# Optimization experiments

Measured on AMD Instinct MI355X. Metric: run time of the kernel, lower is better.

## Reference

```python
import jax, jax.numpy as jnp
import numpy as np

HASH_CODE_LEN = 8  # config['hash_code_len']
EPS = 1e-12

def _l2norm(x):
    n = jnp.sqrt(jnp.sum(x * x, axis=-1, keepdims=True))
    return x / jnp.maximum(n, EPS)

def setup_inputs() -> dict:
    key = jax.random.key(0)
    k1, k2, k3, k4 = jax.random.split(key, 4)
    B, H, S, D = 2, 12, 2048, 64
    Q = jax.random.normal(k1, (B, H, S, D), dtype=jnp.float32)
    K = jax.random.normal(k2, (B, H, S, D), dtype=jnp.float32)
    V = jax.random.normal(k3, (B, H, S, D), dtype=jnp.float32)
    mask = jnp.ones((B, S), dtype=jnp.float32)
    conv_w = jax.random.normal(k4, (H, 1, 3, 1), dtype=jnp.float32)  # depthwise Conv2d weight [H,1,w,1]
    return {"Q": Q, "K": K, "V": V, "mask": mask, "conv_w": conv_w}

def reference(Q, K, V, mask, conv_w):
    B, H, S, D = Q.shape
    # conv branch: depthwise conv over the sequence axis, per head (groups=num_head)
    Vm = V * mask[:, None, :, None]  # [B,H,S,D]
    conv_V = jax.lax.conv_general_dilated(
        Vm, conv_w,
        window_strides=(1, 1),
        padding=[(1, 1), (0, 0)],  # (conv_window//2, 0)
        dimension_numbers=("NCHW", "OIHW", "NCHW"),
        feature_group_count=H,
    )
    # YOSO attention: exact expectation of LSH cumulation.
    # collision prob of unit vectors q,k over hash_code_len bits: (1 - acos(q.k)/pi)^tau
    qn = _l2norm(Q)
    kn = _l2norm(K)
    dots = jnp.einsum("bhsd,bhtd->bhst", qn, kn)
    dots = jnp.clip(dots, -1.0, 1.0)
    W = (1.0 - jnp.arccos(dots) / jnp.pi) ** HASH_CODE_LEN  # [B,H,S,S]
    W = W * mask[:, None, None, :]  # key mask
    X = jnp.einsum("bhst,bhtd->bhsd", W, V)
    X = X * mask[:, None, :, None]  # query mask
    X = _l2norm(X)  # kernel.normalize(X)
    return X + conv_V
```

## Files before the change

### kernel.cpp

```cpp
#include <hip/hip_runtime.h>
#include <hip/hip_bf16.h>
#include <math.h>

#define NB 2
#define NH 12
#define NS 2048
#define ND 64
#define NBH (NB * NH)
#define TILE_USHORT 4096
#define QK_BLOCKS 6144
#define V_BLOCKS (NBH * 32)

typedef __attribute__((ext_vector_type(8))) short short8;
typedef __attribute__((ext_vector_type(4))) float floatx4;
typedef __attribute__((ext_vector_type(2))) float float2v;

__device__ __forceinline__ unsigned short f32_to_bf16_rne(float f) {
  unsigned int u = __float_as_uint(f);
  u += 0x7fffu + ((u >> 16) & 1u);
  return (unsigned short)(u >> 16);
}

__device__ __forceinline__ unsigned int pack_bf16_trunc(float lo, float hi) {
  return __builtin_amdgcn_perm(__float_as_uint(hi), __float_as_uint(lo), 0x07060302);
}

__device__ __forceinline__ float2v mk2(float x) { return (float2v){x, x}; }
__device__ __forceinline__ float2v max2(float2v a, float2v b) {
  return (float2v){fmaxf(a[0], b[0]), fmaxf(a[1], b[1])};
}
__device__ __forceinline__ float2v abs2(float2v a) {
  return (float2v){fabsf(a[0]), fabsf(a[1])};
}

__device__ __forceinline__ float yoso_f_exact(float d) {
  const float c0 = 0.49996030f;
  const float c1 = -0.06751822f;
  const float c2 = 0.02363774f;
  const float c3 = -0.00596174f;
  float a = fminf(fabsf(d), 1.0f);
  float p = fmaf(fmaf(fmaf(c3, a, c2), a, c1), a, c0);
  float u = sqrtf(1.0f - a) * p;
  return (d >= 0.0f) ? (1.0f - u) : u;
}

__device__ __forceinline__ void gload_lds16(const unsigned short* src,
                                            unsigned short* lds_dst) {
  __builtin_amdgcn_global_load_lds(
      (const __attribute__((address_space(1))) unsigned int*)(const void*)src,
      (__attribute__((address_space(3))) unsigned int*)(void*)lds_dst,
      16, 0, 0);
}

__global__ __launch_bounds__(256) void prep_all(
    const float* __restrict__ Q, const float* __restrict__ K,
    const float* __restrict__ V, const float* __restrict__ mask,
    unsigned short* __restrict__ qimg, unsigned short* __restrict__ kimg,
    unsigned short* __restrict__ vimg) {
  int blk = blockIdx.x;
  if (blk < QK_BLOCKS) {
    int row = blk * 16 + (threadIdx.x >> 4);
    int li  = threadIdx.x & 15;
    const float* src = Q;
    unsigned short* dst = qimg;
    if (row >= NBH * NS) { src = K; dst = kimg; row -= NBH * NS; }
    float4 v = *(const float4*)(src + (size_t)row * ND + li * 4);
    float ss = v.x * v.x + v.y * v.y + v.z * v.z + v.w * v.w;
    ss += __shfl_xor(ss, 1, 64);
    ss += __shfl_xor(ss, 2, 64);
    ss += __shfl_xor(ss, 4, 64);
    ss += __shfl_xor(ss, 8, 64);
    float rn = 1.0f / fmaxf(sqrtf(ss), 1e-12f);
    ushort4 o;
    o.x = f32_to_bf16_rne(v.x * rn);
    o.y = f32_to_bf16_rne(v.y * rn);
    o.z = f32_to_bf16_rne(v.z * rn);
    o.w = f32_to_bf16_rne(v.w * rn);
    int bh = row >> 11;
    int s  = row & (NS - 1);
    int kt = s >> 6, r = s & 63;
    int frag = (li >> 3) * 4 + (r >> 4);
    int ln   = ((li >> 1) & 3) * 16 + (r & 15);
    size_t off = (size_t)(bh * 32 + kt) * TILE_USHORT + frag * 512 + ln * 8 + (li & 1) * 4;
    *(ushort4*)(dst + off) = o;
  } else {
    int vb = blk - QK_BLOCKS;
    int bh = vb >> 5, kt = vb & 31, t0 = kt * 64;
    int b  = bh / NH;
    __shared__ float sT[64][65];
    int tid = threadIdx.x;
    int tr = tid >> 2;
    int dc = (tid & 3) * 16;
    float m = mask[b * NS + t0 + tr];
    const float* vp = V + ((size_t)bh * NS + t0 + tr) * ND + dc;
    #pragma unroll
    for (int jj = 0; jj < 16; jj += 4) {
      float4 v = *(const float4*)(vp + jj);
      sT[dc + jj + 0][tr] = v.x * m;
      sT[dc + jj + 1][tr] = v.y * m;
      sT[dc + jj + 2][tr] = v.z * m;
      sT[dc + jj + 3][tr] = v.w * m;
    }
    __syncthreads();
    int dr = tid >> 2;
    unsigned short* op = vimg + (size_t)(bh * 32 + kt) * TILE_USHORT;
    #pragma unroll
    for (int g = 0; g < 2; ++g) {
      int combo = (tid & 3) * 2 + g;
      int kk2 = combo >> 2;
      int qd  = combo & 3;
      uint4 u;
      int tb = kk2 * 32 + qd * 4;
      u.x = (unsigned int)f32_to_bf16_rne(sT[dr][tb + 0]) |
            ((unsigned int)f32_to_bf16_rne(sT[dr][tb + 1]) << 16);
      u.y = (unsigned int)f32_to_bf16_rne(sT[dr][tb + 2]) |
            ((unsigned int)f32_to_bf16_rne(sT[dr][tb + 3]) << 16);
      u.z = (unsigned int)f32_to_bf16_rne(sT[dr][tb + 16]) |
            ((unsigned int)f32_to_bf16_rne(sT[dr][tb + 17]) << 16);
      u.w = (unsigned int)f32_to_bf16_rne(sT[dr][tb + 18]) |
            ((unsigned int)f32_to_bf16_rne(sT[dr][tb + 19]) << 16);
      int frag = kk2 * 4 + (dr >> 4);
      int ln   = qd * 16 + (dr & 15);
      *(uint4*)(op + frag * 512 + ln * 8) = u;
    }
  }
}

__global__ __launch_bounds__(256, 4) void yoso_main(
    const unsigned short* __restrict__ qimg, const unsigned short* __restrict__ kimg,
    const unsigned short* __restrict__ vimg, const float* __restrict__ V,
    const float* __restrict__ mask, const float* __restrict__ conv_w,
    float* __restrict__ out) {
  int bid = blockIdx.x;
  int lid = (bid & 7) * 96 + (bid >> 3);
  int bh = lid >> 5;
  int b  = bh / NH;
  int h  = bh % NH;
  int qt = lid & 31;
  int s0 = qt * 64;

  __shared__ unsigned short stage[2][8192];

  int tid  = threadIdx.x;
  int wv   = tid >> 6;
  int lane = tid & 63;
  int lq   = lane & 15;
  int quad = lane >> 4;

  uint4 qfrag[2];
  {
    const unsigned short* qtile = qimg + (size_t)(bh * 32 + qt) * TILE_USHORT;
    #pragma unroll
    for (int kk = 0; kk < 2; ++kk)
      qfrag[kk] = *(const uint4*)(qtile + (kk * 4 + wv) * 512 + lane * 8);
  }

  float w0 = conv_w[h * 3 + 0], w1 = conv_w[h * 3 + 1], w2 = conv_w[h * 3 + 2];

  floatx4 acc[4];
  #pragma unroll
  for (int fd = 0; fd < 4; ++fd) acc[fd] = (floatx4){0.f, 0.f, 0.f, 0.f};

  const unsigned short* kb  = kimg + (size_t)bh * 32 * TILE_USHORT;
  const unsigned short* vbI = vimg + (size_t)bh * 32 * TILE_USHORT;

  const float P0 = 0.3183098862f;
  const float P1 = 0.0530516477f;
  const float P2 = 0.0238732415f;
  const float P3 = 0.0142098402f;
  const float P4 = 0.0096701727f;
  const float P5 = 0.0071212906f;

  auto stage_tile = [&](int buf, int kt) {
    const unsigned short* ksrc = kb  + (size_t)kt * TILE_USHORT;
    const unsigned short* vsrc = vbI + (size_t)kt * TILE_USHORT;
    #pragma unroll
    for (int c = 0; c < 4; ++c) {
      int region = wv * 4 + c;
      const unsigned short* src = (region < 8) ? (ksrc + region * 512)
                                               : (vsrc + (region - 8) * 512);
      gload_lds16(src + lane * 8, &stage[buf][region * 512]);
    }
  };

  auto compute_tile = [&](const unsigned short* sbuf) {
    uint4 kf[2][4];
    #pragma unroll
    for (int kk = 0; kk < 2; ++kk)
      #pragma unroll
      for (int ft = 0; ft < 4; ++ft)
        kf[kk][ft] = *(const uint4*)(sbuf + (kk * 4 + ft) * 512 + lane * 8);

    floatx4 sc[4];
    #pragma unroll
    for (int ft = 0; ft < 4; ++ft) sc[ft] = (floatx4){0.f, 0.f, 0.f, 0.f};
    #pragma unroll
    for (int kk = 0; kk < 2; ++kk) {
      short8 bq = *(const short8*)&qfrag[kk];
      #pragma unroll
      for (int ft = 0; ft < 4; ++ft)
        sc[ft] = __builtin_amdgcn_mfma_f32_16x16x32_bf16(
            *(const short8*)&kf[kk][ft], bq, sc[ft], 0, 0, 0);
    }

    uint4 vf[2][4];
    #pragma unroll
    for (int kk2 = 0; kk2 < 2; ++kk2)
      #pragma unroll
      for (int fd = 0; fd < 4; ++fd)
        vf[kk2][fd] = *(const uint4*)(sbuf + 4096 + (kk2 * 4 + fd) * 512 + lane * 8);

    {
      float2v mxy = mk2(0.f);
      #pragma unroll
      for (int ft = 0; ft < 4; ++ft) {
        float2v* p = (float2v*)&sc[ft];
        mxy = max2(mxy, max2(abs2(p[0]), abs2(p[1])));
      }
      float mx = fmaxf(mxy[0], mxy[1]);
      if (__builtin_expect(__any(mx > 0.82f), 0)) {
        #pragma unroll
        for (int ft = 0; ft < 4; ++ft)
          #pragma unroll
          for (int r = 0; r < 4; ++r) {
            float f = yoso_f_exact(sc[ft][r]);
            float f2 = f * f;
            float f4 = f2 * f2;
            sc[ft][r] = f4 * f4;
          }
      } else {
        float2v c5 = mk2(P5), c4 = mk2(P4), c3 = mk2(P3), c2 = mk2(P2),
                c1 = mk2(P1), c0 = mk2(P0), hf = mk2(0.5f);
        #pragma unroll
        for (int ft = 0; ft < 4; ++ft) {
          float2v* p = (float2v*)&sc[ft];
          #pragma unroll
          for (int hh = 0; hh < 2; ++hh) {
            float2v d = p[hh];
            float2v y = d * d;
            float2v pp = ((((c5 * y + c4) * y + c3) * y + c2) * y + c1) * y + c0;
            float2v f = pp * d + hf;
            float2v f2 = f * f;
            float2v f4 = f2 * f2;
            p[hh] = f4 * f4;
          }
        }
      }
    }

    #pragma unroll
    for (int kk2 = 0; kk2 < 2; ++kk2) {
      uint4 u;
      u.x = pack_bf16_trunc(sc[2 * kk2][0], sc[2 * kk2][1]);
      u.y = pack_bf16_trunc(sc[2 * kk2][2], sc[2 * kk2][3]);
      u.z = pack_bf16_trunc(sc[2 * kk2 + 1][0], sc[2 * kk2 + 1][1]);
      u.w = pack_bf16_trunc(sc[2 * kk2 + 1][2], sc[2 * kk2 + 1][3]);
      short8 bw = *(short8*)&u;
      #pragma unroll
      for (int fd = 0; fd < 4; ++fd)
        acc[fd] = __builtin_amdgcn_mfma_f32_16x16x32_bf16(
            *(const short8*)&vf[kk2][fd], bw, acc[fd], 0, 0, 0);
    }
  };

  stage_tile(0, 0);
  __syncthreads();
  #pragma unroll 1
  for (int ss = 0; ss < 16; ++ss) {
    int kt = ss * 2;
    stage_tile(1, kt + 1);
    compute_tile(stage[0]);
    __syncthreads();
    if (ss < 15) stage_tile(0, kt + 2);
    compute_tile(stage[1]);
    __syncthreads();
  }

  int s = s0 + wv * 16 + lq;
  float qm  = mask[b * NS + s];
  float qm0 = (s > 0) ? mask[b * NS + s - 1] : 0.f;
  float qm2 = (s < NS - 1) ? mask[b * NS + s + 1] : 0.f;
  float ssum = 0.f;
  #pragma unroll
  for (int fd = 0; fd < 4; ++fd)
    #pragma unroll
    for (int r = 0; r < 4; ++r) {
      float x = acc[fd][r] * qm;
      acc[fd][r] = x;
      ssum += x * x;
    }
  ssum += __shfl_xor(ssum, 16, 64);
  ssum += __shfl_xor(ssum, 32, 64);
  float rn = 1.0f / fmaxf(sqrtf(ssum), 1e-12f);

  const float* vfull = V + ((size_t)bh * NS + s) * ND;
  #pragma unroll
  for (int fd = 0; fd < 4; ++fd) {
    int d = fd * 16 + quad * 4;
    float4 vc1 = *(const float4*)(vfull + d);
    float4 cv;
    cv.x = w1 * vc1.x * qm; cv.y = w1 * vc1.y * qm;
    cv.z = w1 * vc1.z * qm; cv.w = w1 * vc1.w * qm;
    if (s > 0) {
      float4 vc0 = *(const float4*)(vfull - ND + d);
      cv.x += w0 * vc0.x * qm0; cv.y += w0 * vc0.y * qm0;
      cv.z += w0 * vc0.z * qm0; cv.w += w0 * vc0.w * qm0;
    }
    if (s < NS - 1) {
      float4 vc2 = *(const float4*)(vfull + ND + d);
      cv.x += w2 * vc2.x * qm2; cv.y += w2 * vc2.y * qm2;
      cv.z += w2 * vc2.z * qm2; cv.w += w2 * vc2.w * qm2;
    }
    float4 o;
    o.x = acc[fd][0] * rn + cv.x;
    o.y = acc[fd][1] * rn + cv.y;
    o.z = acc[fd][2] * rn + cv.z;
    o.w = acc[fd][3] * rn + cv.w;
    *(float4*)(out + ((size_t)bh * NS + s) * ND + d) = o;
  }
}

extern "C" void kernel_launch(void* const* d_in, const int* in_sizes, int n_in,
                              void* d_out, int out_size, void* d_ws, size_t ws_size,
                              hipStream_t stream) {
  const float* Q      = (const float*)d_in[0];
  const float* K      = (const float*)d_in[1];
  const float* V      = (const float*)d_in[2];
  const float* mask   = (const float*)d_in[3];
  const float* conv_w = (const float*)d_in[4];
  float* out = (float*)d_out;

  const size_t seg = (size_t)NBH * NS * ND * sizeof(unsigned short);
  unsigned short* qimg = (unsigned short*)d_ws;
  unsigned short* kimg = (unsigned short*)((char*)d_ws + seg);
  unsigned short* vimg = (unsigned short*)((char*)d_ws + 2 * seg);

  prep_all<<<QK_BLOCKS + V_BLOCKS, 256, 0, stream>>>(Q, K, V, mask, qimg, kimg, vimg);
  yoso_main<<<NBH * 32, 256, 0, stream>>>(qimg, kimg, vimg, V, mask, conv_w, out);
}
```

Before: 142.5 us.

## Split key tiles across wave pairs and read V fragments directly from global

Work is repartitioned so each wave handles two 16-row query fragments and half of the key tiles, with the two key-parity halves reduced through shared memory at the end. Only K is staged into LDS, two tiles at a time. V fragments are now loaded straight from global memory instead of through LDS. The aim is to reuse each K fragment across two query fragments and halve the number of loop-iteration barriers. The cost is higher register pressure (launch bounds lowered from 4 to 3 blocks per CU), uncoalesced-latency exposure on the direct V loads, and an extra cross-wave reduction in the epilogue.

```diff
diff --git a/kernel.cpp b/kernel.cpp
--- a/kernel.cpp
+++ b/kernel.cpp
@@ -126,7 +126,7 @@
   }
 }
 
-__global__ __launch_bounds__(256, 4) void yoso_main(
+__global__ __launch_bounds__(256, 3) void yoso_main(
     const unsigned short* __restrict__ qimg, const unsigned short* __restrict__ kimg,
     const unsigned short* __restrict__ vimg, const float* __restrict__ V,
     const float* __restrict__ mask, const float* __restrict__ conv_w,
@@ -139,27 +139,33 @@
   int qt = lid & 31;
   int s0 = qt * 64;
 
-  __shared__ unsigned short stage[2][8192];
+  __shared__ unsigned short kbuf[4][4096];
 
   int tid  = threadIdx.x;
   int wv   = tid >> 6;
   int lane = tid & 63;
   int lq   = lane & 15;
   int quad = lane >> 4;
-
-  uint4 qfrag[2];
+  int qs   = wv & 1;
+  int kp   = wv >> 1;
+
+  uint4 qfrag[2][2];
   {
     const unsigned short* qtile = qimg + (size_t)(bh * 32 + qt) * TILE_USHORT;
     #pragma unroll
-    for (int kk = 0; kk < 2; ++kk)
-      qfrag[kk] = *(const uint4*)(qtile + (kk * 4 + wv) * 512 + lane * 8);
+    for (int j = 0; j < 2; ++j)
+      #pragma unroll
+      for (int kk = 0; kk < 2; ++kk)
+        qfrag[j][kk] = *(const uint4*)(qtile + (kk * 4 + qs * 2 + j) * 512 + lane * 8);
   }
 
   float w0 = conv_w[h * 3 + 0], w1 = conv_w[h * 3 + 1], w2 = conv_w[h * 3 + 2];
 
-  floatx4 acc[4];
+  floatx4 acc[2][4];
   #pragma unroll
-  for (int fd = 0; fd < 4; ++fd) acc[fd] = (floatx4){0.f, 0.f, 0.f, 0.f};
+  for (int j = 0; j < 2; ++j)
+    #pragma unroll
+    for (int fd = 0; fd < 4; ++fd) acc[j][fd] = (floatx4){0.f, 0.f, 0.f, 0.f};
 
   const unsigned short* kb  = kimg + (size_t)bh * 32 * TILE_USHORT;
   const unsigned short* vbI = vimg + (size_t)bh * 32 * TILE_USHORT;
@@ -171,152 +177,193 @@
   const float P4 = 0.0096701727f;
   const float P5 = 0.0071212906f;
 
-  auto stage_tile = [&](int buf, int kt) {
-    const unsigned short* ksrc = kb  + (size_t)kt * TILE_USHORT;
-    const unsigned short* vsrc = vbI + (size_t)kt * TILE_USHORT;
+  auto stage_pair = [&](int pb, int t0) {
     #pragma unroll
     for (int c = 0; c < 4; ++c) {
       int region = wv * 4 + c;
-      const unsigned short* src = (region < 8) ? (ksrc + region * 512)
-                                               : (vsrc + (region - 8) * 512);
-      gload_lds16(src + lane * 8, &stage[buf][region * 512]);
+      int tsel   = region >> 3;
+      int piece  = region & 7;
+      gload_lds16(kb + (size_t)(t0 + tsel) * TILE_USHORT + piece * 512 + lane * 8,
+                  &kbuf[pb + tsel][piece * 512]);
     }
   };
 
-  auto compute_tile = [&](const unsigned short* sbuf) {
+  stage_pair(0, 0);
+  __syncthreads();
+
+  #pragma unroll 1
+  for (int r = 0; r < 16; ++r) {
+    int pb = (r & 1) * 2;
+    if (r < 15) stage_pair(2 - pb, 2 * r + 2);
+
+    int kt = 2 * r + kp;
+    const unsigned short* sb = kbuf[pb + kp];
+
     uint4 kf[2][4];
     #pragma unroll
     for (int kk = 0; kk < 2; ++kk)
       #pragma unroll
       for (int ft = 0; ft < 4; ++ft)
-        kf[kk][ft] = *(const uint4*)(sbuf + (kk * 4 + ft) * 512 + lane * 8);
-
-    floatx4 sc[4];
-    #pragma unroll
-    for (int ft = 0; ft < 4; ++ft) sc[ft] = (floatx4){0.f, 0.f, 0.f, 0.f};
+        kf[kk][ft] = *(const uint4*)(sb + (kk * 4 + ft) * 512 + lane * 8);
+
+    floatx4 sc[2][4];
+    #pragma unroll
+    for (int j = 0; j < 2; ++j)
+      #pragma unroll
+      for (int ft = 0; ft < 4; ++ft) sc[j][ft] = (floatx4){0.f, 0.f, 0.f, 0.f};
     #pragma unroll
     for (int kk = 0; kk < 2; ++kk) {
-      short8 bq = *(const short8*)&qfrag[kk];
-      #pragma unroll
-      for (int ft = 0; ft < 4; ++ft)
-        sc[ft] = __builtin_amdgcn_mfma_f32_16x16x32_bf16(
-            *(const short8*)&kf[kk][ft], bq, sc[ft], 0, 0, 0);
-    }
-
+      #pragma unroll
+      for (int j = 0; j < 2; ++j) {
+        short8 bq = *(const short8*)&qfrag[j][kk];
+        #pragma unroll
+        for (int ft = 0; ft < 4; ++ft)
+          sc[j][ft] = __builtin_amdgcn_mfma_f32_16x16x32_bf16(
+              *(const short8*)&kf[kk][ft], bq, sc[j][ft], 0, 0, 0);
+      }
+    }
+
+    const unsigned short* vtile = vbI + (size_t)kt * TILE_USHORT;
     uint4 vf[2][4];
     #pragma unroll
     for (int kk2 = 0; kk2 < 2; ++kk2)
       #pragma unroll
       for (int fd = 0; fd < 4; ++fd)
-        vf[kk2][fd] = *(const uint4*)(sbuf + 4096 + (kk2 * 4 + fd) * 512 + lane * 8);
+        vf[kk2][fd] = *(const uint4*)(vtile + (kk2 * 4 + fd) * 512 + lane * 8);
 
     {
       float2v mxy = mk2(0.f);
       #pragma unroll
-      for (int ft = 0; ft < 4; ++ft) {
-        float2v* p = (float2v*)&sc[ft];
-        mxy = max2(mxy, max2(abs2(p[0]), abs2(p[1])));
-      }
+      for (int j = 0; j < 2; ++j)
+        #pragma unroll
+        for (int ft = 0; ft < 4; ++ft) {
+          float2v* p = (float2v*)&sc[j][ft];
+          mxy = max2(mxy, max2(abs2(p[0]), abs2(p[1])));
+        }
       float mx = fmaxf(mxy[0], mxy[1]);
       if (__builtin_expect(__any(mx > 0.82f), 0)) {
         #pragma unroll
-        for (int ft = 0; ft < 4; ++ft)
+        for (int j = 0; j < 2; ++j)
           #pragma unroll
-          for (int r = 0; r < 4; ++r) {
-            float f = yoso_f_exact(sc[ft][r]);
-            float f2 = f * f;
-            float f4 = f2 * f2;
-            sc[ft][r] = f4 * f4;
-          }
+          for (int ft = 0; ft < 4; ++ft)
+            #pragma unroll
+            for (int r2 = 0; r2 < 4; ++r2) {
+              float f = yoso_f_exact(sc[j][ft][r2]);
+              float f2 = f * f;
+              float f4 = f2 * f2;
+              sc[j][ft][r2] = f4 * f4;
+            }
       } else {
         float2v c5 = mk2(P5), c4 = mk2(P4), c3 = mk2(P3), c2 = mk2(P2),
                 c1 = mk2(P1), c0 = mk2(P0), hf = mk2(0.5f);
         #pragma unroll
-        for (int ft = 0; ft < 4; ++ft) {
-          float2v* p = (float2v*)&sc[ft];
+        for (int j = 0; j < 2; ++j)
           #pragma unroll
-          for (int hh = 0; hh < 2; ++hh) {
-            float2v d = p[hh];
-            float2v y = d * d;
-            float2v pp = ((((c5 * y + c4) * y + c3) * y + c2) * y + c1) * y + c0;
-            float2v f = pp * d + hf;
-            float2v f2 = f * f;
-            float2v f4 = f2 * f2;
-            p[hh] = f4 * f4;
+          for (int ft = 0; ft < 4; ++ft) {
+            float2v* p = (float2v*)&sc[j][ft];
+            #pragma unroll
+            for (int hh = 0; hh < 2; ++hh) {
+              float2v d = p[hh];
+              float2v y = d * d;
+              float2v pp = ((((c5 * y + c4) * y + c3) * y + c2) * y + c1) * y + c0;
+              float2v f = pp * d + hf;
+              float2v f2 = f * f;
+              float2v f4 = f2 * f2;
+              p[hh] = f4 * f4;
+            }
           }
+      }
+    }
+
+    #pragma unroll
+    for (int j = 0; j < 2; ++j) {
+      #pragma unroll
+      for (int kk2 = 0; kk2 < 2; ++kk2) {
+        uint4 u;
+        u.x = pack_bf16_trunc(sc[j][2 * kk2][0], sc[j][2 * kk2][1]);
+        u.y = pack_bf16_trunc(sc[j][2 * kk2][2], sc[j][2 * kk2][3]);
+        u.z = pack_bf16_trunc(sc[j][2 * kk2 + 1][0], sc[j][2 * kk2 + 1][1]);
+        u.w = pack_bf16_trunc(sc[j][2 * kk2 + 1][2], sc[j][2 * kk2 + 1][3]);
+        short8 bw = *(short8*)&u;
+        #pragma unroll
+        for (int fd = 0; fd < 4; ++fd)
+          acc[j][fd] = __builtin_amdgcn_mfma_f32_16x16x32_bf16(
+              *(const short8*)&vf[kk2][fd], bw, acc[j][fd], 0, 0, 0);
+      }
+    }
+
+    __syncthreads();
+  }
+
+  float* xch = (float*)&kbuf[0][0];
+  if (kp == 1) {
+    #pragma unroll
+    for (int j = 0; j < 2; ++j) {
+      float* wr = xch + (qs * 2 + j) * 1088;
+      #pragma unroll
+      for (int fd = 0; fd < 4; ++fd)
+        #pragma unroll
+        for (int r2 = 0; r2 < 4; ++r2)
+          wr[lq * 68 + fd * 16 + quad * 4 + r2] = acc[j][fd][r2];
+    }
+  }
+  __syncthreads();
+  if (kp == 0) {
+    #pragma unroll
+    for (int j = 0; j < 2; ++j) {
+      const float* rd = xch + (qs * 2 + j) * 1088;
+      #pragma unroll
+      for (int fd = 0; fd < 4; ++fd)
+        #pragma unroll
+        for (int r2 = 0; r2 < 4; ++r2)
+          acc[j][fd][r2] += rd[lq * 68 + fd * 16 + quad * 4 + r2];
+    }
+
+    #pragma unroll
+    for (int j = 0; j < 2; ++j) {
+      int s = s0 + qs * 32 + j * 16 + lq;
+      float qm  = mask[b * NS + s];
+      float qm0 = (s > 0) ? mask[b * NS + s - 1] : 0.f;
+      float qm2 = (s < NS - 1) ? mask[b * NS + s + 1] : 0.f;
+      float ssum = 0.f;
+      #pragma unroll
+      for (int fd = 0; fd < 4; ++fd)
+        #pragma unroll
+        for (int r2 = 0; r2 < 4; ++r2) {
+          float x = acc[j][fd][r2] * qm;
+          acc[j][fd][r2] = x;
+          ssum += x * x;
         }
+      ssum += __shfl_xor(ssum, 16, 64);
+      ssum += __shfl_xor(ssum, 32, 64);
+      float rn = 1.0f / fmaxf(sqrtf(ssum), 1e-12f);
+
+      const float* vfull = V + ((size_t)bh * NS + s) * ND;
+      #pragma unroll
+      for (int fd = 0; fd < 4; ++fd) {
+        int d = fd * 16 + quad * 4;
+        float4 vc1 = *(const float4*)(vfull + d);
+        float4 cv;
+        cv.x = w1 * vc1.x * qm; cv.y = w1 * vc1.y * qm;
+        cv.z = w1 * vc1.z * qm; cv.w = w1 * vc1.w * qm;
+        if (s > 0) {
+          float4 vc0 = *(const float4*)(vfull - ND + d);
+          cv.x += w0 * vc0.x * qm0; cv.y += w0 * vc0.y * qm0;
+          cv.z += w0 * vc0.z * qm0; cv.w += w0 * vc0.w * qm0;
+        }
+        if (s < NS - 1) {
+          float4 vc2 = *(const float4*)(vfull + ND + d);
+          cv.x += w2 * vc2.x * qm2; cv.y += w2 * vc2.y * qm2;
+          cv.z += w2 * vc2.z * qm2; cv.w += w2 * vc2.w * qm2;
+        }
+        float4 o;
+        o.x = acc[j][fd][0] * rn + cv.x;
+        o.y = acc[j][fd][1] * rn + cv.y;
+        o.z = acc[j][fd][2] * rn + cv.z;
+        o.w = acc[j][fd][3] * rn + cv.w;
+        *(float4*)(out + ((size_t)bh * NS + s) * ND + d) = o;
       }
     }
-
-    #pragma unroll
-    for (int kk2 = 0; kk2 < 2; ++kk2) {
-      uint4 u;
-      u.x = pack_bf16_trunc(sc[2 * kk2][0], sc[2 * kk2][1]);
-      u.y = pack_bf16_trunc(sc[2 * kk2][2], sc[2 * kk2][3]);
-      u.z = pack_bf16_trunc(sc[2 * kk2 + 1][0], sc[2 * kk2 + 1][1]);
-      u.w = pack_bf16_trunc(sc[2 * kk2 + 1][2], sc[2 * kk2 + 1][3]);
-      short8 bw = *(short8*)&u;
-      #pragma unroll
-      for (int fd = 0; fd < 4; ++fd)
-        acc[fd] = __builtin_amdgcn_mfma_f32_16x16x32_bf16(
-            *(const short8*)&vf[kk2][fd], bw, acc[fd], 0, 0, 0);
-    }
-  };
-
-  stage_tile(0, 0);
-  __syncthreads();
-  #pragma unroll 1
-  for (int ss = 0; ss < 16; ++ss) {
-    int kt = ss * 2;
-    stage_tile(1, kt + 1);
-    compute_tile(stage[0]);
-    __syncthreads();
-    if (ss < 15) stage_tile(0, kt + 2);
-    compute_tile(stage[1]);
-    __syncthreads();
-  }
-
-  int s = s0 + wv * 16 + lq;
-  float qm  = mask[b * NS + s];
-  float qm0 = (s > 0) ? mask[b * NS + s - 1] : 0.f;
-  float qm2 = (s < NS - 1) ? mask[b * NS + s + 1] : 0.f;
-  float ssum = 0.f;
-  #pragma unroll
-  for (int fd = 0; fd < 4; ++fd)
-    #pragma unroll
-    for (int r = 0; r < 4; ++r) {
-      float x = acc[fd][r] * qm;
-      acc[fd][r] = x;
-      ssum += x * x;
-    }
-  ssum += __shfl_xor(ssum, 16, 64);
-  ssum += __shfl_xor(ssum, 32, 64);
-  float rn = 1.0f / fmaxf(sqrtf(ssum), 1e-12f);
-
-  const float* vfull = V + ((size_t)bh * NS + s) * ND;
-  #pragma unroll
-  for (int fd = 0; fd < 4; ++fd) {
-    int d = fd * 16 + quad * 4;
-    float4 vc1 = *(const float4*)(vfull + d);
-    float4 cv;
-    cv.x = w1 * vc1.x * qm; cv.y = w1 * vc1.y * qm;
-    cv.z = w1 * vc1.z * qm; cv.w = w1 * vc1.w * qm;
-    if (s > 0) {
-      float4 vc0 = *(const float4*)(vfull - ND + d);
-      cv.x += w0 * vc0.x * qm0; cv.y += w0 * vc0.y * qm0;
-      cv.z += w0 * vc0.z * qm0; cv.w += w0 * vc0.w * qm0;
-    }
-    if (s < NS - 1) {
-      float4 vc2 = *(const float4*)(vfull + ND + d);
-      cv.x += w2 * vc2.x * qm2; cv.y += w2 * vc2.y * qm2;
-      cv.z += w2 * vc2.z * qm2; cv.w += w2 * vc2.w * qm2;
-    }
-    float4 o;
-    o.x = acc[fd][0] * rn + cv.x;
-    o.y = acc[fd][1] * rn + cv.y;
-    o.z = acc[fd][2] * rn + cv.z;
-    o.w = acc[fd][3] * rn + cv.w;
-    *(float4*)(out + ((size_t)bh * NS + s) * ND + d) = o;
   }
 }
 
```

New measurement: 140.6 us. Within noise of the previous version (-1.3%).
